# Performance work log

Hardware: AMD Instinct MI355X
Metric: run time of the kernel (lower is better)

Reference implementation:

```python
import jax, jax.numpy as jnp
import numpy as np


def setup_inputs() -> dict:
    key = jax.random.key(0)
    B, N = 4, 32768
    xyz = jax.random.normal(key, (B, N, 3), dtype=jnp.float32)
    return {"xyz": xyz, "K": 16, "nqueries": 2048}


def reference(xyz, K, nqueries):
    # xyz: (b, n, 3). Deterministic strided pick of nqueries query points
    # (stand-in for the KD-tree's distance-pick sampling), then brute-force KNN.
    b, n, _ = xyz.shape
    stride = n // nqueries
    q_idx = jnp.arange(nqueries) * stride          # (nq,)
    pts = xyz[:, q_idx, :]                          # (b, nq, 3) sampled query points
    # pairwise squared distances (b, nq, n)
    d = jnp.sum((pts[:, :, None, :] - xyz[:, None, :, :]) ** 2, axis=-1)
    _, idx = jax.lax.top_k(-d, K)                   # (b, nq, K) nearest-neighbor indices
    idx = idx.astype(jnp.int64)[..., None]          # (b, nq, K, 1) matches expand_dims(..., 3)
    return idx, pts
```

## Files before the change

### kernel.cpp

```cpp
#include <hip/hip_runtime.h>
#include <stdint.h>

#define NPTS  32768
#define NQ    2048
#define KNN   16
#define NB    4
#define TS    2048
#define BLOCK 512
#define WPB   8

typedef const __attribute__((address_space(1))) char glds_src_t;
typedef __attribute__((address_space(3))) char glds_dst_t;

__device__ __forceinline__ float2 pk_add(float2 a, float2 b) {
    float2 r;
    asm("v_pk_add_f32 %0, %1, %2" : "=v"(r) : "v"(a), "v"(b));
    return r;
}
__device__ __forceinline__ float2 pk_mul(float2 a, float2 b) {
    float2 r;
    asm("v_pk_mul_f32 %0, %1, %2" : "=v"(r) : "v"(a), "v"(b));
    return r;
}
__device__ __forceinline__ int dpp_shr1_i(int x) {
    return __builtin_amdgcn_update_dpp(x, x, 0x111, 0xf, 0xf, false);
}
__device__ __forceinline__ float dpp_shr1_f(float x) {
    int r = dpp_shr1_i(__float_as_int(x));
    return __int_as_float(r);
}
__device__ __forceinline__ float readlane_f(float x, int l) {
    return __int_as_float(__builtin_amdgcn_readlane(__float_as_int(x), l));
}

template <int T>
__device__ __forceinline__ void insert_all(float d, int p, int lane,
                                           float& ld, int& li, float& tau)
{
    unsigned long long rem = __ballot(d <= tau);
    while (rem) {
        const int srcl = __ffsll(rem) - 1;
        const float wd = readlane_f(d, srcl);
        const int   wi = __builtin_amdgcn_readlane(p, srcl);
        const bool less = (ld < wd) || (ld == wd && li < wi);
        const unsigned long long lm = __ballot(less);
        const int pos = __popc((unsigned)((lm >> (16 * T)) & 0xffffull));
        const float pld = dpp_shr1_f(ld);
        const int   pli = dpp_shr1_i(li);
        if ((lane >> 4) == T) {
            const int gl = lane & 15;
            if (gl == pos)      { ld = wd;  li = wi;  }
            else if (gl > pos)  { ld = pld; li = pli; }
        }
        tau = readlane_f(ld, 16 * T + 15);
        rem &= rem - 1;
        if (rem) rem &= __ballot(d <= tau);
    }
}

__global__ __launch_bounds__(BLOCK) void knn_kernel(const float* __restrict__ xyz,
                                                    float* __restrict__ out_idx,
                                                    float* __restrict__ out_pts)
{
    __shared__ float lds[TS * 3];

    const int tid  = threadIdx.x;
    const int lane = tid & 63;
    const int wv   = tid >> 6;
    const int w    = blockIdx.x * WPB + wv;
    const int b    = w >> 10;
    const int pr   = w & 1023;
    const size_t base = (size_t)b * NPTS * 3;

    const int qp0 = pr << 5;
    const float qx0 = xyz[base + 3 * qp0 + 0];
    const float qy0 = xyz[base + 3 * qp0 + 1];
    const float qz0 = xyz[base + 3 * qp0 + 2];
    const float qx1 = xyz[base + 3 * qp0 + 48];
    const float qy1 = xyz[base + 3 * qp0 + 49];
    const float qz1 = xyz[base + 3 * qp0 + 50];

    const int g0 = b * NQ + (pr << 1);
    if (lane == 0) {
        out_pts[3 * g0 + 0] = qx0;
        out_pts[3 * g0 + 1] = qy0;
        out_pts[3 * g0 + 2] = qz0;
        out_pts[3 * g0 + 3] = qx1;
        out_pts[3 * g0 + 4] = qy1;
        out_pts[3 * g0 + 5] = qz1;
    }

    const float2 nqx = make_float2(-qx0, -qx1);
    const float2 nqy = make_float2(-qy0, -qy1);
    const float2 nqz = make_float2(-qz0, -qz1);

    float ld = __builtin_inff();  int li = 0x7fffffff;
    float tau0 = __builtin_inff(), tau1 = __builtin_inff();

    const float4* lp = (const float4*)lds + 3 * lane;

    for (int tile = 0; tile < NPTS; tile += TS) {
        __syncthreads();
        {
            glds_src_t* gsrc = (glds_src_t*)(xyz + base + (size_t)tile * 3);
            glds_dst_t* ldst = (glds_dst_t*)lds;
            #pragma unroll
            for (int c = 0; c < 3; ++c)
                __builtin_amdgcn_global_load_lds(
                    (const __attribute__((address_space(1))) void*)(gsrc + 16 * (BLOCK * c + tid)),
                    (__attribute__((address_space(3))) void*)(ldst + 16 * (BLOCK * c + tid)),
                    16, 0, 0);
        }
        __syncthreads();

        #pragma unroll
        for (int k = 0; k < TS / 256; ++k) {
            const float4 A = lp[192 * k + 0];
            const float4 Bv = lp[192 * k + 1];
            const float4 Cv = lp[192 * k + 2];
            const float px[4] = { A.x,  A.w,  Bv.z, Cv.y };
            const float py[4] = { A.y,  Bv.x, Bv.w, Cv.z };
            const float pz[4] = { A.z,  Bv.y, Cv.x, Cv.w };

            float d0[4], d1[4];
            bool any = false;
            #pragma unroll
            for (int j = 0; j < 4; ++j) {
                const float2 dx = pk_add(make_float2(px[j], px[j]), nqx);
                const float2 dy = pk_add(make_float2(py[j], py[j]), nqy);
                const float2 dz = pk_add(make_float2(pz[j], pz[j]), nqz);
                const float2 s  = pk_add(pk_add(pk_mul(dx, dx), pk_mul(dy, dy)),
                                         pk_mul(dz, dz));
                d0[j] = s.x;  d1[j] = s.y;
                any = any | (d0[j] <= tau0) | (d1[j] <= tau1);
            }
            if (__ballot(any)) {
                const int pb = tile + 256 * k + 4 * lane;
                #pragma unroll
                for (int j = 0; j < 4; ++j) {
                    insert_all<0>(d0[j], pb + j, lane, ld, li, tau0);
                    insert_all<1>(d1[j], pb + j, lane, ld, li, tau1);
                }
            }
        }
    }

    if (lane < 2 * KNN) {
        out_idx[(size_t)g0 * KNN + lane] = (float)li;
    }
}

extern "C" void kernel_launch(void* const* d_in, const int* in_sizes, int n_in,
                              void* d_out, int out_size, void* d_ws, size_t ws_size,
                              hipStream_t stream) {
    const float* xyz = (const float*)d_in[0];
    float* out = (float*)d_out;
    float* out_idx = out;
    float* out_pts = out + (size_t)NB * NQ * KNN;

    const int blocks = (NB * NQ / 2) / WPB;
    knn_kernel<<<blocks, BLOCK, 0, stream>>>(xyz, out_idx, out_pts);
}
```

Baseline: 222.9 us.

## Split point range across two waves per query pair, read directly from global

Each query pair is now handled by two wavefronts, each scanning half of the point cloud, and the two partial top-16 lists are merged through a small LDS rank-count step. The LDS tiling and barriers are removed: points are read straight from global memory with float4 loads and rely on the cache. The screening pass uses fused multiply-add distances compared against a slightly inflated threshold, and exact distances are recomputed only for candidates that pass, to keep ordering identical. This raises parallelism and removes block-wide synchronisation, at the cost of an extra merge step and a dependence on cache hit rate for the point data.

New measurement: 232.2 us. 4.2% more time.

```diff
diff --git a/kernel.cpp b/kernel.cpp
--- a/kernel.cpp
+++ b/kernel.cpp
@@ -5,29 +5,14 @@
 #define NQ    2048
 #define KNN   16
 #define NB    4
-#define TS    2048
-#define BLOCK 512
-#define WPB   8
+#define BLOCK 256
+#define HALF  16384
 
-typedef const __attribute__((address_space(1))) char glds_src_t;
-typedef __attribute__((address_space(3))) char glds_dst_t;
-
-__device__ __forceinline__ float2 pk_add(float2 a, float2 b) {
-    float2 r;
-    asm("v_pk_add_f32 %0, %1, %2" : "=v"(r) : "v"(a), "v"(b));
-    return r;
-}
-__device__ __forceinline__ float2 pk_mul(float2 a, float2 b) {
-    float2 r;
-    asm("v_pk_mul_f32 %0, %1, %2" : "=v"(r) : "v"(a), "v"(b));
-    return r;
-}
 __device__ __forceinline__ int dpp_shr1_i(int x) {
     return __builtin_amdgcn_update_dpp(x, x, 0x111, 0xf, 0xf, false);
 }
 __device__ __forceinline__ float dpp_shr1_f(float x) {
-    int r = dpp_shr1_i(__float_as_int(x));
-    return __int_as_float(r);
+    return __int_as_float(dpp_shr1_i(__float_as_int(x)));
 }
 __device__ __forceinline__ float readlane_f(float x, int l) {
     return __int_as_float(__builtin_amdgcn_readlane(__float_as_int(x), l));
@@ -35,7 +20,7 @@
 
 template <int T>
 __device__ __forceinline__ void insert_all(float d, int p, int lane,
-                                           float& ld, int& li, float& tau)
+                                           float& ld, int& li, float& tau, float& tg)
 {
     unsigned long long rem = __ballot(d <= tau);
     while (rem) {
@@ -53,23 +38,27 @@
             else if (gl > pos)  { ld = pld; li = pli; }
         }
         tau = readlane_f(ld, 16 * T + 15);
+        tg  = tau * 1.00001f;
         rem &= rem - 1;
         if (rem) rem &= __ballot(d <= tau);
     }
 }
 
-__global__ __launch_bounds__(BLOCK) void knn_kernel(const float* __restrict__ xyz,
-                                                    float* __restrict__ out_idx,
-                                                    float* __restrict__ out_pts)
+__global__ __launch_bounds__(BLOCK, 6) void knn_kernel(const float* __restrict__ xyz,
+                                                       float* __restrict__ out_idx,
+                                                       float* __restrict__ out_pts)
 {
-    __shared__ float lds[TS * 3];
+    __shared__ float d_buf[2][2][2][KNN];
+    __shared__ int   i_buf[2][2][2][KNN];
 
-    const int tid  = threadIdx.x;
-    const int lane = tid & 63;
-    const int wv   = tid >> 6;
-    const int w    = blockIdx.x * WPB + wv;
-    const int b    = w >> 10;
-    const int pr   = w & 1023;
+    const int tid   = threadIdx.x;
+    const int lane  = tid & 63;
+    const int wv    = tid >> 6;
+    const int pairw = wv >> 1;
+    const int h     = wv & 1;
+    const int qpg   = blockIdx.x * 2 + pairw;
+    const int b     = qpg >> 10;
+    const int pr    = qpg & 1023;
     const size_t base = (size_t)b * NPTS * 3;
 
     const int qp0 = pr << 5;
@@ -81,7 +70,7 @@
     const float qz1 = xyz[base + 3 * qp0 + 50];
 
     const int g0 = b * NQ + (pr << 1);
-    if (lane == 0) {
+    if (h == 0 && lane == 0) {
         out_pts[3 * g0 + 0] = qx0;
         out_pts[3 * g0 + 1] = qy0;
         out_pts[3 * g0 + 2] = qz0;
@@ -90,63 +79,95 @@
         out_pts[3 * g0 + 5] = qz1;
     }
 
-    const float2 nqx = make_float2(-qx0, -qx1);
-    const float2 nqy = make_float2(-qy0, -qy1);
-    const float2 nqz = make_float2(-qz0, -qz1);
-
     float ld = __builtin_inff();  int li = 0x7fffffff;
     float tau0 = __builtin_inff(), tau1 = __builtin_inff();
+    float tg0  = __builtin_inff(), tg1  = __builtin_inff();
 
-    const float4* lp = (const float4*)lds + 3 * lane;
+    const float4* lp = (const float4*)(xyz + base) + h * (HALF * 3 / 4) + 3 * lane;
 
-    for (int tile = 0; tile < NPTS; tile += TS) {
-        __syncthreads();
+    #pragma unroll 2
+    for (int k = 0; k < HALF / 256; ++k) {
+        const float4 A  = lp[192 * k + 0];
+        const float4 Bv = lp[192 * k + 1];
+        const float4 Cv = lp[192 * k + 2];
+        const float px[4] = { A.x,  A.w,  Bv.z, Cv.y };
+        const float py[4] = { A.y,  Bv.x, Bv.w, Cv.z };
+        const float pz[4] = { A.z,  Bv.y, Cv.x, Cv.w };
+
+        unsigned long long m00, m01, m02, m03, m10, m11, m12, m13;
         {
-            glds_src_t* gsrc = (glds_src_t*)(xyz + base + (size_t)tile * 3);
-            glds_dst_t* ldst = (glds_dst_t*)lds;
-            #pragma unroll
-            for (int c = 0; c < 3; ++c)
-                __builtin_amdgcn_global_load_lds(
-                    (const __attribute__((address_space(1))) void*)(gsrc + 16 * (BLOCK * c + tid)),
-                    (__attribute__((address_space(3))) void*)(ldst + 16 * (BLOCK * c + tid)),
-                    16, 0, 0);
+            float dx, dy, dz, g;
+            dx = px[0] - qx0; dy = py[0] - qy0; dz = pz[0] - qz0;
+            g = __fmaf_rn(dz, dz, __fmaf_rn(dy, dy, __fmul_rn(dx, dx)));
+            m00 = __ballot(g <= tg0);
+            dx = px[1] - qx0; dy = py[1] - qy0; dz = pz[1] - qz0;
+            g = __fmaf_rn(dz, dz, __fmaf_rn(dy, dy, __fmul_rn(dx, dx)));
+            m01 = __ballot(g <= tg0);
+            dx = px[2] - qx0; dy = py[2] - qy0; dz = pz[2] - qz0;
+            g = __fmaf_rn(dz, dz, __fmaf_rn(dy, dy, __fmul_rn(dx, dx)));
+            m02 = __ballot(g <= tg0);
+            dx = px[3] - qx0; dy = py[3] - qy0; dz = pz[3] - qz0;
+            g = __fmaf_rn(dz, dz, __fmaf_rn(dy, dy, __fmul_rn(dx, dx)));
+            m03 = __ballot(g <= tg0);
+            dx = px[0] - qx1; dy = py[0] - qy1; dz = pz[0] - qz1;
+            g = __fmaf_rn(dz, dz, __fmaf_rn(dy, dy, __fmul_rn(dx, dx)));
+            m10 = __ballot(g <= tg1);
+            dx = px[1] - qx1; dy = py[1] - qy1; dz = pz[1] - qz1;
+            g = __fmaf_rn(dz, dz, __fmaf_rn(dy, dy, __fmul_rn(dx, dx)));
+            m11 = __ballot(g <= tg1);
+            dx = px[2] - qx1; dy = py[2] - qy1; dz = pz[2] - qz1;
+            g = __fmaf_rn(dz, dz, __fmaf_rn(dy, dy, __fmul_rn(dx, dx)));
+            m12 = __ballot(g <= tg1);
+            dx = px[3] - qx1; dy = py[3] - qy1; dz = pz[3] - qz1;
+            g = __fmaf_rn(dz, dz, __fmaf_rn(dy, dy, __fmul_rn(dx, dx)));
+            m13 = __ballot(g <= tg1);
         }
-        __syncthreads();
 
-        #pragma unroll
-        for (int k = 0; k < TS / 256; ++k) {
-            const float4 A = lp[192 * k + 0];
-            const float4 Bv = lp[192 * k + 1];
-            const float4 Cv = lp[192 * k + 2];
-            const float px[4] = { A.x,  A.w,  Bv.z, Cv.y };
-            const float py[4] = { A.y,  Bv.x, Bv.w, Cv.z };
-            const float pz[4] = { A.z,  Bv.y, Cv.x, Cv.w };
-
-            float d0[4], d1[4];
-            bool any = false;
-            #pragma unroll
-            for (int j = 0; j < 4; ++j) {
-                const float2 dx = pk_add(make_float2(px[j], px[j]), nqx);
-                const float2 dy = pk_add(make_float2(py[j], py[j]), nqy);
-                const float2 dz = pk_add(make_float2(pz[j], pz[j]), nqz);
-                const float2 s  = pk_add(pk_add(pk_mul(dx, dx), pk_mul(dy, dy)),
-                                         pk_mul(dz, dz));
-                d0[j] = s.x;  d1[j] = s.y;
-                any = any | (d0[j] <= tau0) | (d1[j] <= tau1);
-            }
-            if (__ballot(any)) {
-                const int pb = tile + 256 * k + 4 * lane;
-                #pragma unroll
-                for (int j = 0; j < 4; ++j) {
-                    insert_all<0>(d0[j], pb + j, lane, ld, li, tau0);
-                    insert_all<1>(d1[j], pb + j, lane, ld, li, tau1);
+        if (m00 | m01 | m02 | m03 | m10 | m11 | m12 | m13) {
+            const int pb = h * HALF + (k << 8) + 4 * lane;
+            #define SLOW(mask, J, T, QX, QY, QZ, TAU, TGV)                          \
+                if (mask) {                                                         \
+                    const float dx = __fadd_rn(px[J], -(QX));                       \
+                    const float dy = __fadd_rn(py[J], -(QY));                       \
+                    const float dz = __fadd_rn(pz[J], -(QZ));                       \
+                    const float d  = __fadd_rn(                                     \
+                        __fadd_rn(__fmul_rn(dx, dx), __fmul_rn(dy, dy)),            \
+                        __fmul_rn(dz, dz));                                         \
+                    insert_all<T>(d, pb + J, lane, ld, li, TAU, TGV);               \
                 }
-            }
+            SLOW(m00, 0, 0, qx0, qy0, qz0, tau0, tg0)
+            SLOW(m01, 1, 0, qx0, qy0, qz0, tau0, tg0)
+            SLOW(m02, 2, 0, qx0, qy0, qz0, tau0, tg0)
+            SLOW(m03, 3, 0, qx0, qy0, qz0, tau0, tg0)
+            SLOW(m10, 0, 1, qx1, qy1, qz1, tau1, tg1)
+            SLOW(m11, 1, 1, qx1, qy1, qz1, tau1, tg1)
+            SLOW(m12, 2, 1, qx1, qy1, qz1, tau1, tg1)
+            SLOW(m13, 3, 1, qx1, qy1, qz1, tau1, tg1)
+            #undef SLOW
         }
     }
 
-    if (lane < 2 * KNN) {
-        out_idx[(size_t)g0 * KNN + lane] = (float)li;
+    if (lane < 32) {
+        const int t = lane >> 4;
+        d_buf[pairw][t][h][lane & 15] = ld;
+        i_buf[pairw][t][h][lane & 15] = li;
+    }
+    __syncthreads();
+
+    if (h == 0) {
+        const int t = lane >> 5;
+        const int s = lane & 31;
+        const float d = d_buf[pairw][t][s >> 4][s & 15];
+        const int   i = i_buf[pairw][t][s >> 4][s & 15];
+        int cnt = 0;
+        #pragma unroll
+        for (int r = 0; r < 32; ++r) {
+            const float od = d_buf[pairw][t][r >> 4][r & 15];
+            const int   oi = i_buf[pairw][t][r >> 4][r & 15];
+            cnt += ((od < d) || (od == d && oi < i)) ? 1 : 0;
+        }
+        if (cnt < KNN)
+            out_idx[(size_t)(g0 + t) * KNN + cnt] = (float)i;
     }
 }
 
@@ -158,6 +179,6 @@
     float* out_idx = out;
     float* out_pts = out + (size_t)NB * NQ * KNN;
 
-    const int blocks = (NB * NQ / 2) / WPB;
+    const int blocks = (NB * NQ / 2) / 2;
     knn_kernel<<<blocks, BLOCK, 0, stream>>>(xyz, out_idx, out_pts);
 }
```

## Stream points from global via register double-buffering with FMA prefilter

Applied to the files above, without the earlier changes.

Drops the LDS tile staging and block-wide syncthreads. Each lane now loads 8 points straight from global memory into registers, double-buffered across iterations. Candidates are screened with a cheap FMA distance against a slightly inflated threshold, and the exact distance is recomputed only for ballots that pass. The block shrinks to 256 threads with a launch-bounds occupancy hint. This removes barrier stalls and LDS traffic, at the cost of more register pressure and relying on L2 reuse across waves.

New measurement: 195.7 us. 12.2% less time.

```diff
diff --git a/kernel.cpp b/kernel.cpp
--- a/kernel.cpp
+++ b/kernel.cpp
@@ -5,29 +5,16 @@
 #define NQ    2048
 #define KNN   16
 #define NB    4
-#define TS    2048
-#define BLOCK 512
-#define WPB   8
+#define BLOCK 256
+#define WPB   4
+#define PPL   8
+#define ITERS (NPTS / (64 * PPL))
 
-typedef const __attribute__((address_space(1))) char glds_src_t;
-typedef __attribute__((address_space(3))) char glds_dst_t;
-
-__device__ __forceinline__ float2 pk_add(float2 a, float2 b) {
-    float2 r;
-    asm("v_pk_add_f32 %0, %1, %2" : "=v"(r) : "v"(a), "v"(b));
-    return r;
-}
-__device__ __forceinline__ float2 pk_mul(float2 a, float2 b) {
-    float2 r;
-    asm("v_pk_mul_f32 %0, %1, %2" : "=v"(r) : "v"(a), "v"(b));
-    return r;
-}
 __device__ __forceinline__ int dpp_shr1_i(int x) {
     return __builtin_amdgcn_update_dpp(x, x, 0x111, 0xf, 0xf, false);
 }
 __device__ __forceinline__ float dpp_shr1_f(float x) {
-    int r = dpp_shr1_i(__float_as_int(x));
-    return __int_as_float(r);
+    return __int_as_float(dpp_shr1_i(__float_as_int(x)));
 }
 __device__ __forceinline__ float readlane_f(float x, int l) {
     return __int_as_float(__builtin_amdgcn_readlane(__float_as_int(x), l));
@@ -35,7 +22,7 @@
 
 template <int T>
 __device__ __forceinline__ void insert_all(float d, int p, int lane,
-                                           float& ld, int& li, float& tau)
+                                           float& ld, int& li, float& tau, float& tg)
 {
     unsigned long long rem = __ballot(d <= tau);
     while (rem) {
@@ -53,17 +40,77 @@
             else if (gl > pos)  { ld = pld; li = pli; }
         }
         tau = readlane_f(ld, 16 * T + 15);
+        tg  = tau * 1.00001f;
         rem &= rem - 1;
         if (rem) rem &= __ballot(d <= tau);
     }
 }
 
-__global__ __launch_bounds__(BLOCK) void knn_kernel(const float* __restrict__ xyz,
-                                                    float* __restrict__ out_idx,
-                                                    float* __restrict__ out_pts)
+__device__ __forceinline__ void load6(float4 dst[6], const float4* p) {
+    #pragma unroll
+    for (int t = 0; t < 6; ++t) dst[t] = p[t];
+}
+
+__device__ __forceinline__ void step(const float4 c[6], int pb, int lane,
+                                     float qx0, float qy0, float qz0,
+                                     float qx1, float qy1, float qz1,
+                                     float& ld, int& li,
+                                     float& tau0, float& tau1,
+                                     float& tg0, float& tg1)
 {
-    __shared__ float lds[TS * 3];
+    float px[PPL], py[PPL], pz[PPL];
+    px[0] = c[0].x; py[0] = c[0].y; pz[0] = c[0].z;
+    px[1] = c[0].w; py[1] = c[1].x; pz[1] = c[1].y;
+    px[2] = c[1].z; py[2] = c[1].w; pz[2] = c[2].x;
+    px[3] = c[2].y; py[3] = c[2].z; pz[3] = c[2].w;
+    px[4] = c[3].x; py[4] = c[3].y; pz[4] = c[3].z;
+    px[5] = c[3].w; py[5] = c[4].x; pz[5] = c[4].y;
+    px[6] = c[4].z; py[6] = c[4].w; pz[6] = c[5].x;
+    px[7] = c[5].y; py[7] = c[5].z; pz[7] = c[5].w;
 
+    unsigned long long m0[PPL], m1[PPL], any = 0;
+    #pragma unroll
+    for (int j = 0; j < PPL; ++j) {
+        const float ax = px[j] - qx0, ay = py[j] - qy0, az = pz[j] - qz0;
+        const float g0 = __fmaf_rn(az, az, __fmaf_rn(ay, ay, __fmul_rn(ax, ax)));
+        m0[j] = __ballot(g0 <= tg0);
+        const float bx = px[j] - qx1, by = py[j] - qy1, bz = pz[j] - qz1;
+        const float g1 = __fmaf_rn(bz, bz, __fmaf_rn(by, by, __fmul_rn(bx, bx)));
+        m1[j] = __ballot(g1 <= tg1);
+        any |= m0[j] | m1[j];
+    }
+    if (any) {
+        #pragma unroll
+        for (int j = 0; j < PPL; ++j) {
+            if (m0[j]) {
+                const float dx = __fadd_rn(px[j], -qx0);
+                const float dy = __fadd_rn(py[j], -qy0);
+                const float dz = __fadd_rn(pz[j], -qz0);
+                const float d  = __fadd_rn(
+                    __fadd_rn(__fmul_rn(dx, dx), __fmul_rn(dy, dy)),
+                    __fmul_rn(dz, dz));
+                insert_all<0>(d, pb + j, lane, ld, li, tau0, tg0);
+            }
+        }
+        #pragma unroll
+        for (int j = 0; j < PPL; ++j) {
+            if (m1[j]) {
+                const float dx = __fadd_rn(px[j], -qx1);
+                const float dy = __fadd_rn(py[j], -qy1);
+                const float dz = __fadd_rn(pz[j], -qz1);
+                const float d  = __fadd_rn(
+                    __fadd_rn(__fmul_rn(dx, dx), __fmul_rn(dy, dy)),
+                    __fmul_rn(dz, dz));
+                insert_all<1>(d, pb + j, lane, ld, li, tau1, tg1);
+            }
+        }
+    }
+}
+
+__global__ __launch_bounds__(BLOCK, 4) void knn_kernel(const float* __restrict__ xyz,
+                                                       float* __restrict__ out_idx,
+                                                       float* __restrict__ out_pts)
+{
     const int tid  = threadIdx.x;
     const int lane = tid & 63;
     const int wv   = tid >> 6;
@@ -90,59 +137,23 @@
         out_pts[3 * g0 + 5] = qz1;
     }
 
-    const float2 nqx = make_float2(-qx0, -qx1);
-    const float2 nqy = make_float2(-qy0, -qy1);
-    const float2 nqz = make_float2(-qz0, -qz1);
-
     float ld = __builtin_inff();  int li = 0x7fffffff;
     float tau0 = __builtin_inff(), tau1 = __builtin_inff();
+    float tg0  = __builtin_inff(), tg1  = __builtin_inff();
 
-    const float4* lp = (const float4*)lds + 3 * lane;
+    const float4* lp = (const float4*)(xyz + base) + 6 * lane;
 
-    for (int tile = 0; tile < NPTS; tile += TS) {
-        __syncthreads();
-        {
-            glds_src_t* gsrc = (glds_src_t*)(xyz + base + (size_t)tile * 3);
-            glds_dst_t* ldst = (glds_dst_t*)lds;
-            #pragma unroll
-            for (int c = 0; c < 3; ++c)
-                __builtin_amdgcn_global_load_lds(
-                    (const __attribute__((address_space(1))) void*)(gsrc + 16 * (BLOCK * c + tid)),
-                    (__attribute__((address_space(3))) void*)(ldst + 16 * (BLOCK * c + tid)),
-                    16, 0, 0);
-        }
-        __syncthreads();
-
-        #pragma unroll
-        for (int k = 0; k < TS / 256; ++k) {
-            const float4 A = lp[192 * k + 0];
-            const float4 Bv = lp[192 * k + 1];
-            const float4 Cv = lp[192 * k + 2];
-            const float px[4] = { A.x,  A.w,  Bv.z, Cv.y };
-            const float py[4] = { A.y,  Bv.x, Bv.w, Cv.z };
-            const float pz[4] = { A.z,  Bv.y, Cv.x, Cv.w };
-
-            float d0[4], d1[4];
-            bool any = false;
-            #pragma unroll
-            for (int j = 0; j < 4; ++j) {
-                const float2 dx = pk_add(make_float2(px[j], px[j]), nqx);
-                const float2 dy = pk_add(make_float2(py[j], py[j]), nqy);
-                const float2 dz = pk_add(make_float2(pz[j], pz[j]), nqz);
-                const float2 s  = pk_add(pk_add(pk_mul(dx, dx), pk_mul(dy, dy)),
-                                         pk_mul(dz, dz));
-                d0[j] = s.x;  d1[j] = s.y;
-                any = any | (d0[j] <= tau0) | (d1[j] <= tau1);
-            }
-            if (__ballot(any)) {
-                const int pb = tile + 256 * k + 4 * lane;
-                #pragma unroll
-                for (int j = 0; j < 4; ++j) {
-                    insert_all<0>(d0[j], pb + j, lane, ld, li, tau0);
-                    insert_all<1>(d1[j], pb + j, lane, ld, li, tau1);
-                }
-            }
-        }
+    float4 A[6], Bf[6];
+    load6(A, lp);
+    for (int k = 0; k < ITERS; k += 2) {
+        load6(Bf, lp + 384);
+        step(A, (k << 9) + PPL * lane, lane,
+             qx0, qy0, qz0, qx1, qy1, qz1, ld, li, tau0, tau1, tg0, tg1);
+        if (k + 2 < ITERS)
+            load6(A, lp + 768);
+        step(Bf, ((k + 1) << 9) + PPL * lane, lane,
+             qx0, qy0, qz0, qx1, qy1, qz1, ld, li, tau0, tau1, tg0, tg1);
+        lp += 768;
     }
 
     if (lane < 2 * KNN) {
```
